# Performance work log

Measured on AMD Instinct MI355X. Metric: run time of the kernel, lower is better.

## Reference

```python
import jax, jax.numpy as jnp
import numpy as np

N = {'QENT': 20000, 'CENT': 50000, 'SPAN': 40000, 'SENT': 40000}
E = 250000
IN_DIM, HID = 256, 128
NEG_SLOPE = 0.2  # GATConv default negative_slope
RELS = [('QENT', 'SPAN'), ('QENT', 'SENT'), ('CENT', 'SENT'), ('SPAN', 'CENT'), ('CENT', 'CENT')]
ENAMES = ['e_qent_span', 'e_qent_sent', 'e_cent_sent', 'e_span_cent', 'e_cent_cooccur']


def setup_inputs() -> dict:
    key = jax.random.key(0)
    ks = jax.random.split(key, 20)
    inp = {}
    for i, t in enumerate(['QENT', 'CENT', 'SPAN', 'SENT']):
        inp['x_' + t] = jax.random.normal(ks[i], (N[t], IN_DIM), jnp.float32)
    for i, (nm, (s, d)) in enumerate(zip(ENAMES, RELS)):
        k1, k2 = jax.random.split(ks[4 + i])
        src = jax.random.randint(k1, (E,), 0, N[s])
        dst = jax.random.randint(k2, (E,), 0, N[d])
        inp[nm] = jnp.stack([src, dst]).astype(jnp.int32)
    inp['lin_W'] = jax.random.normal(ks[10], (4, IN_DIM, HID), jnp.float32) / np.sqrt(IN_DIM).astype(np.float32)
    inp['lin_b'] = jnp.zeros((4, HID), jnp.float32)
    inp['conv_Ws'] = jax.random.normal(ks[11], (2, 5, HID, HID), jnp.float32) / np.sqrt(HID).astype(np.float32)
    inp['conv_Wd'] = jax.random.normal(ks[12], (2, 5, HID, HID), jnp.float32) / np.sqrt(HID).astype(np.float32)
    inp['conv_as'] = jax.random.normal(ks[13], (2, 5, HID), jnp.float32) / np.sqrt(HID).astype(np.float32)
    inp['conv_ad'] = jax.random.normal(ks[14], (2, 5, HID), jnp.float32) / np.sqrt(HID).astype(np.float32)
    inp['conv_b'] = jnp.zeros((2, 5, HID), jnp.float32)
    inp['out_W'] = jax.random.normal(ks[15], (HID, 1), jnp.float32) / np.sqrt(HID).astype(np.float32)
    inp['out_b'] = jnp.zeros((1,), jnp.float32)
    return inp


def _gat(x_src, x_dst, edge, Ws, Wd, a_s, a_d, b, n_dst):
    """PyG GATConv, heads=1, concat=True, add_self_loops=False, bipartite lin_src/lin_dst."""
    hs = x_src @ Ws                       # [Ns, H]
    hd = x_dst @ Wd                       # [Nd, H]
    src, dst = edge[0], edge[1]
    e = jax.nn.leaky_relu((hs @ a_s)[src] + (hd @ a_d)[dst], NEG_SLOPE)  # [E]
    m = jax.ops.segment_max(e, dst, num_segments=n_dst)
    m = jnp.where(jnp.isfinite(m), m, 0.0)
    ex = jnp.exp(e - m[dst])
    denom = jax.ops.segment_sum(ex, dst, num_segments=n_dst)
    alpha = ex / (denom[dst] + 1e-16)     # segment softmax (PyG adds 1e-16)
    out = jax.ops.segment_sum(alpha[:, None] * hs[src], dst, num_segments=n_dst)
    return out + b


def _forward(x_QENT, x_CENT, x_SPAN, x_SENT,
             e_qent_span, e_qent_sent, e_cent_sent, e_span_cent, e_cent_cooccur,
             lin_W, lin_b, conv_Ws, conv_Wd, conv_as, conv_ad, conv_b, out_W, out_b):
    # per-type input projection (pyg Linear has bias)
    x = {'QENT': x_QENT @ lin_W[0] + lin_b[0],
         'CENT': x_CENT @ lin_W[1] + lin_b[1],
         'SPAN': x_SPAN @ lin_W[2] + lin_b[2],
         'SENT': x_SENT @ lin_W[3] + lin_b[3]}
    for l in range(2):
        p = lambda r: (conv_Ws[l, r], conv_Wd[l, r], conv_as[l, r], conv_ad[l, r], conv_b[l, r])
        span = _gat(x['QENT'], x['SPAN'], e_qent_span, *p(0), N['SPAN'])
        sent = (_gat(x['QENT'], x['SENT'], e_qent_sent, *p(1), N['SENT'])
                + _gat(x['CENT'], x['SENT'], e_cent_sent, *p(2), N['SENT']))  # HeteroConv aggr='sum'
        cent = (_gat(x['SPAN'], x['CENT'], e_span_cent, *p(3), N['CENT'])
                + _gat(x['CENT'], x['CENT'], e_cent_cooccur, *p(4), N['CENT']))
        x = {'QENT': x['QENT'],  # QENT has no incoming edges; carried through so layer 2 can use it as source
             'SPAN': jax.nn.relu(span),
             'SENT': jax.nn.relu(sent),
             'CENT': jax.nn.relu(cent)}
    return (x['SPAN'] @ out_W + out_b)[:, 0]  # squeeze(-1) -> [N_SPAN]


def reference(x_QENT, x_CENT, x_SPAN, x_SENT,
              e_qent_span, e_qent_sent, e_cent_sent, e_span_cent, e_cent_cooccur,
              lin_W, lin_b, conv_Ws, conv_Wd, conv_as, conv_ad, conv_b, out_W, out_b):
    return _forward(x_QENT, x_CENT, x_SPAN, x_SENT,
                    e_qent_span, e_qent_sent, e_cent_sent, e_span_cent, e_cent_cooccur,
                    lin_W, lin_b, conv_Ws, conv_Wd, conv_as, conv_ad, conv_b, out_W, out_b)
```

## Files before the change

### kernel.cpp

```cpp
#include <hip/hip_runtime.h>
#include <hip/hip_fp16.h>

#define IN_DIM 256
#define HID 128
#define ELLW 16
#define OVF_CAP 32768

using bf16x8 = __attribute__((ext_vector_type(8))) short;
using f32x4 = __attribute__((ext_vector_type(4))) float;

struct h8 { __half2 a, b, c, d; };

__device__ __forceinline__ unsigned short f2bf(float f) {
    unsigned u = __float_as_uint(f);
    u += 0x7fffu + ((u >> 16) & 1u);
    return (unsigned short)(u >> 16);
}

template <int CTRL>
__device__ __forceinline__ float dpp_rot(float x) {
    return __int_as_float(
        __builtin_amdgcn_update_dpp(0, __float_as_int(x), CTRL, 0xf, 0xf, false));
}
__device__ __forceinline__ float rsum16(float x) {
    x += dpp_rot<0x121>(x);
    x += dpp_rot<0x122>(x);
    x += dpp_rot<0x124>(x);
    x += dpp_rot<0x128>(x);
    return x;
}
__device__ __forceinline__ float rmax16(float x) {
    x = fmaxf(x, dpp_rot<0x121>(x));
    x = fmaxf(x, dpp_rot<0x122>(x));
    x = fmaxf(x, dpp_rot<0x124>(x));
    x = fmaxf(x, dpp_rot<0x128>(x));
    return x;
}

__device__ __forceinline__ float lrelu(float t) { return t > 0.f ? t : 0.2f * t; }

__device__ __forceinline__ void accum8(f32x4& a0, f32x4& a1, float a, const h8& hv) {
    const float2 f0 = __half22float2(hv.a);
    const float2 f1 = __half22float2(hv.b);
    const float2 f2 = __half22float2(hv.c);
    const float2 f3 = __half22float2(hv.d);
    a0[0] += a * f0.x; a0[1] += a * f0.y;
    a0[2] += a * f1.x; a0[3] += a * f1.y;
    a1[0] += a * f2.x; a1[1] += a * f2.y;
    a1[2] += a * f3.x; a1[3] += a * f3.y;
}

__device__ __forceinline__ float epilogue16(const f32x4& a0, const f32x4& a1,
                                            const float* __restrict__ bias,
                                            const float* __restrict__ dvec, int sl) {
    const f32x4 bb0 = *reinterpret_cast<const f32x4*>(bias + sl * 8);
    const f32x4 bb1 = *reinterpret_cast<const f32x4*>(bias + sl * 8 + 4);
    const f32x4 d0 = *reinterpret_cast<const f32x4*>(dvec + sl * 8);
    const f32x4 d1 = *reinterpret_cast<const f32x4*>(dvec + sl * 8 + 4);
    float q = 0.f;
#pragma unroll
    for (int i = 0; i < 4; ++i) {
        q += fmaxf(a0[i] + bb0[i], 0.f) * d0[i];
        q += fmaxf(a1[i] + bb1[i], 0.f) * d1[i];
    }
    return rsum16(q);
}

__global__ __launch_bounds__(256) void setup_k(const float* __restrict__ lin_W,
                                               const float* __restrict__ lin_b,
                                               const float* __restrict__ conv_Ws,
                                               const float* __restrict__ Wd,
                                               const float* __restrict__ adv,
                                               short* __restrict__ wt0,
                                               short* __restrict__ wt1,
                                               float* __restrict__ bc,
                                               float* __restrict__ wd_out,
                                               float* __restrict__ v2,
                                               float* __restrict__ c2,
                                               int* __restrict__ deg,
                                               int* __restrict__ ell,
                                               int* __restrict__ ovf_cnt, int NS, int zd) {
    const int b = blockIdx.x;
    if (b < 256) {
        const int idx = b * 256 + threadIdx.x;
        const int l = idx >> 15;
        const int rem = idx & 32767;
        const int k = rem >> 7;
        const int n = rem & 127;
        const float* lw = lin_W + (size_t)k * HID;
        const float* cw = conv_Ws + (size_t)(l * 5) * HID * HID + n;
        float s = 0.f;
#pragma unroll 4
        for (int m = 0; m < HID; ++m) s += lw[m] * cw[(size_t)m * HID];
        short* wt = l ? wt1 : wt0;
        wt[((k >> 3) << 10) + (n << 3) + (k & 7)] = (short)f2bf(s);
    } else if (b == 256) {
        const int t = threadIdx.x;
        const int l = t >> 7;
        const int n = t & 127;
        const float* cw = conv_Ws + (size_t)(l * 5) * HID * HID + n;
        float s = 0.f;
#pragma unroll 4
        for (int m = 0; m < HID; ++m) s += lin_b[m] * cw[(size_t)m * HID];
        bc[t] = s;
        if (t == 0) ovf_cnt[0] = 0;
    } else if (b == 257) {
        __shared__ float wd1s[HID];
        const int t = threadIdx.x;
        const int l = t >> 7, j = t & 127;
        const float* w = Wd + ((size_t)(l * 5) * HID + j) * HID;
        const float* a = adv + (size_t)(l * 5) * HID;
        float s = 0.f;
        for (int k = 0; k < HID; k += 4) {
            const float4 wv = *reinterpret_cast<const float4*>(w + k);
            const float4 av = *reinterpret_cast<const float4*>(a + k);
            s += wv.x * av.x + wv.y * av.y + wv.z * av.z + wv.w * av.w;
        }
        wd_out[t] = s;
        if (l == 0) wd1s[j] = s;
        __syncthreads();
        const float* wr = lin_W + 2 * (size_t)IN_DIM * HID + (size_t)t * HID;
        float p = 0.f;
        for (int k = 0; k < HID; k += 4) {
            const float4 wv = *reinterpret_cast<const float4*>(wr + k);
            p += wv.x * wd1s[k] + wv.y * wd1s[k + 1] + wv.z * wd1s[k + 2] +
                 wv.w * wd1s[k + 3];
        }
        v2[t] = p;
        if (t == 0) {
            const float* br = lin_b + 2 * HID;
            float q = 0.f;
            for (int k = 0; k < HID; ++k) q += br[k] * wd1s[k];
            c2[0] = q;
        }
    } else if (b < 258 + zd) {
        const int i4 = ((b - 258) * 256 + threadIdx.x) * 4;
        if (i4 + 4 <= NS) {
            *reinterpret_cast<int4*>(deg + i4) = make_int4(0, 0, 0, 0);
        } else {
            for (int i = i4; i < NS; ++i) deg[i] = 0;
        }
    } else {
        const int total = NS * ELLW;
        const int i4 = ((b - 258 - zd) * 256 + threadIdx.x) * 4;
        if (i4 + 4 <= total) *reinterpret_cast<int4*>(ell + i4) = make_int4(0, 0, 0, 0);
    }
}

__global__ __launch_bounds__(256) void build_gemm_k(
    const int* __restrict__ src, const int* __restrict__ dst, int E,
    int* __restrict__ deg, int* __restrict__ ell, int2* __restrict__ ovf,
    int* __restrict__ ovf_cnt, const float* __restrict__ A,
    const short* __restrict__ Wt0, const short* __restrict__ Wt1,
    const float* __restrict__ bc, __half* __restrict__ hs,
    float2* __restrict__ as12, const float* __restrict__ a1v,
    const float* __restrict__ a2v, int N, int eb) {
    if ((int)blockIdx.x < eb) {
        const int e = blockIdx.x * 256 + threadIdx.x;
        if (e < E) {
            const int d = dst[e], s = src[e];
            const int pos = atomicAdd(deg + d, 1);
            if (pos < ELLW) {
                ell[(size_t)d * ELLW + pos] = s;
            } else {
                const int oi = atomicAdd(ovf_cnt, 1);
                if (oi < OVF_CAP) ovf[oi] = make_int2(d, s);
            }
        }
        return;
    }
    const int bid = (int)blockIdx.x - eb;
    const int tid = threadIdx.x;
    const int w = tid >> 6;
    const int lane = tid & 63;
    const int m16 = lane & 15;
    const int kg = lane >> 4;

    const int arow = bid * 64 + w * 16 + m16;
    const bool ok = arow < N;

    f32x4 acc[16];
#pragma unroll
    for (int j = 0; j < 16; ++j) acc[j] = (f32x4){0.f, 0.f, 0.f, 0.f};

    for (int k0 = 0; k0 < IN_DIM; k0 += 32) {
        bf16x8 af = {0, 0, 0, 0, 0, 0, 0, 0};
        if (ok) {
            const float* ap = A + (size_t)arow * IN_DIM + k0 + kg * 8;
            const float4 f0 = *reinterpret_cast<const float4*>(ap);
            const float4 f1 = *reinterpret_cast<const float4*>(ap + 4);
            af[0] = (short)f2bf(f0.x); af[1] = (short)f2bf(f0.y);
            af[2] = (short)f2bf(f0.z); af[3] = (short)f2bf(f0.w);
            af[4] = (short)f2bf(f1.x); af[5] = (short)f2bf(f1.y);
            af[6] = (short)f2bf(f1.z); af[7] = (short)f2bf(f1.w);
        }
        const int boff = ((k0 >> 3) + kg) << 10;
        const short* b0 = Wt0 + boff;
        const short* b1 = Wt1 + boff;
#pragma unroll
        for (int j = 0; j < 8; ++j) {
            const bf16x8 bf0 = *reinterpret_cast<const bf16x8*>(b0 + ((j * 16 + m16) << 3));
            acc[j] = __builtin_amdgcn_mfma_f32_16x16x32_bf16(af, bf0, acc[j], 0, 0, 0);
            const bf16x8 bf1 = *reinterpret_cast<const bf16x8*>(b1 + ((j * 16 + m16) << 3));
            acc[j + 8] = __builtin_amdgcn_mfma_f32_16x16x32_bf16(af, bf1, acc[j + 8], 0, 0, 0);
        }
    }

    const int rbase = bid * 64 + w * 16 + kg * 4;
    float p1[4] = {0.f, 0.f, 0.f, 0.f};
    float p2[4] = {0.f, 0.f, 0.f, 0.f};
#pragma unroll
    for (int j = 0; j < 8; ++j) {
        const int col = j * 16 + m16;
        const float b0v = bc[col];
        const float b1v = bc[128 + col];
        const float a1 = a1v[col];
        const float a2 = a2v[col];
        const int so = j * 32 + ((m16 >> 3) << 4) + (m16 & 7);
#pragma unroll
        for (int r = 0; r < 4; ++r) {
            const int row = rbase + r;
            const float v1 = acc[j][r] + b0v;
            const float v2v = acc[j + 8][r] + b1v;
            if (row < N) {
                hs[(size_t)row * 256 + so] = __float2half(v1);
                hs[(size_t)row * 256 + so + 8] = __float2half(v2v);
            }
            p1[r] += v1 * a1;
            p2[r] += v2v * a2;
        }
    }
#pragma unroll
    for (int r = 0; r < 4; ++r) {
        p1[r] = rsum16(p1[r]);
        p2[r] = rsum16(p2[r]);
    }
    if (m16 == 0)
#pragma unroll
        for (int r = 0; r < 4; ++r) {
            const int row = rbase + r;
            if (row < N) as12[row] = make_float2(p1[r], p2[r]);
        }
}

__global__ __launch_bounds__(256, 4) void gat_fused_k(
    const int* __restrict__ deg_arr, const int* __restrict__ ell,
    const int2* __restrict__ ovf, const int* __restrict__ ovf_cnt_p,
    const float* __restrict__ x_span, const float* __restrict__ v2,
    const float* __restrict__ c2, const float2* __restrict__ as12,
    const __half* __restrict__ hs, const float* __restrict__ b1,
    const float* __restrict__ wd2v, const float* __restrict__ b2,
    const float* __restrict__ outW, const float* __restrict__ outb,
    float* __restrict__ out, int Ndst) {
    const int row = (blockIdx.x * blockDim.x + threadIdx.x) >> 6;
    const int lane = threadIdx.x & 63;
    const int sl = lane & 15;
    const int eg = lane >> 4;
    if (row >= Ndst) return;

    const int deg = deg_arr[row];
    const int ce = ell[(size_t)row * ELLW + sl];
    const float2 asv = as12[ce];

    const float4 xv = *reinterpret_cast<const float4*>(x_span + (size_t)row * IN_DIM +
                                                       lane * 4);
    const float4 vv = *reinterpret_cast<const float4*>(v2 + lane * 4);
    float p = xv.x * vv.x + xv.y * vv.y + xv.z * vv.z + xv.w * vv.w;
    p = rsum16(p);
    p += __shfl_xor(p, 16, 64);
    p += __shfl_xor(p, 32, 64);
    const float ad1 = p + c2[0];

    if (deg <= ELLW) {
        const float ex1 = (sl < deg) ? __expf(lrelu(asv.x + ad1)) : 0.f;
        const float al1 = ex1 / (rsum16(ex1) + 1e-16f);

        f32x4 a0 = {0.f, 0.f, 0.f, 0.f}, a1 = {0.f, 0.f, 0.f, 0.f};
        h8 h2s[4];
#pragma unroll
        for (int r = 0; r < 4; ++r) {
            if (r * 4 < deg) {
                const int e = r * 4 + eg;
                const int s = __shfl(ce, e, 64);
                const float a = __shfl(al1, e, 64);
                const __half* hb = hs + (size_t)s * 256 + sl * 16;
                const h8 hv1 = *reinterpret_cast<const h8*>(hb);
                h2s[r] = *reinterpret_cast<const h8*>(hb + 8);
                accum8(a0, a1, a, hv1);
            }
        }
#pragma unroll
        for (int i = 0; i < 4; ++i) {
            a0[i] += __shfl_xor(a0[i], 16, 64);
            a0[i] += __shfl_xor(a0[i], 32, 64);
            a1[i] += __shfl_xor(a1[i], 16, 64);
            a1[i] += __shfl_xor(a1[i], 32, 64);
        }
        const float ad2 = epilogue16(a0, a1, b1, wd2v, sl);

        const float ex2 = (sl < deg) ? __expf(lrelu(asv.y + ad2)) : 0.f;
        const float al2 = ex2 / (rsum16(ex2) + 1e-16f);

        f32x4 b0 = {0.f, 0.f, 0.f, 0.f}, b1v = {0.f, 0.f, 0.f, 0.f};
#pragma unroll
        for (int r = 0; r < 4; ++r) {
            if (r * 4 < deg) {
                const float a = __shfl(al2, r * 4 + eg, 64);
                accum8(b0, b1v, a, h2s[r]);
            }
        }
#pragma unroll
        for (int i = 0; i < 4; ++i) {
            b0[i] += __shfl_xor(b0[i], 16, 64);
            b0[i] += __shfl_xor(b0[i], 32, 64);
            b1v[i] += __shfl_xor(b1v[i], 16, 64);
            b1v[i] += __shfl_xor(b1v[i], 32, 64);
        }
        const float q = epilogue16(b0, b1v, b2, outW, sl);
        if (lane == 0) out[row] = q + outb[0];
    } else {
        int oc = *ovf_cnt_p;
        if (oc > OVF_CAP) oc = OVF_CAP;
        float ad = ad1;
#pragma unroll
        for (int layer = 0; layer < 2; ++layer) {
            const float ac = layer ? asv.y : asv.x;
            const int ho = layer ? 8 : 0;
            const float* bias = layer ? b2 : b1;
            const float* dvec = layer ? outW : wd2v;

            float te = lrelu(ac + ad);
            float m = rmax16(te);
            for (int i = 0; i < oc; ++i) {
                const int2 o = ovf[i];
                if (o.x == row) {
                    const float2 oas = as12[o.y];
                    m = fmaxf(m, lrelu((layer ? oas.y : oas.x) + ad));
                }
            }
            const float ex = __expf(te - m);
            float dsum = rsum16(ex);
            for (int i = 0; i < oc; ++i) {
                const int2 o = ovf[i];
                if (o.x == row) {
                    const float2 oas = as12[o.y];
                    dsum += __expf(lrelu((layer ? oas.y : oas.x) + ad) - m);
                }
            }
            const float inv = 1.f / (dsum + 1e-16f);
            const float al = ex * inv;

            f32x4 acc0 = {0.f, 0.f, 0.f, 0.f}, acc1 = {0.f, 0.f, 0.f, 0.f};
            for (int i = 0; i < 16; ++i) {
                const int s = __shfl(ce, i, 64);
                float a = __shfl(al, i, 64);
                if (eg != 0) a = 0.f;
                const h8 hv =
                    *reinterpret_cast<const h8*>(hs + (size_t)s * 256 + sl * 16 + ho);
                accum8(acc0, acc1, a, hv);
            }
            for (int i = 0; i < oc; ++i) {
                const int2 o = ovf[i];
                if (o.x == row && eg == 0) {
                    const float2 oas = as12[o.y];
                    const float a = __expf(lrelu((layer ? oas.y : oas.x) + ad) - m) * inv;
                    const h8 hv =
                        *reinterpret_cast<const h8*>(hs + (size_t)o.y * 256 + sl * 16 + ho);
                    accum8(acc0, acc1, a, hv);
                }
            }
#pragma unroll
            for (int i = 0; i < 4; ++i) {
                acc0[i] += __shfl_xor(acc0[i], 16, 64);
                acc0[i] += __shfl_xor(acc0[i], 32, 64);
                acc1[i] += __shfl_xor(acc1[i], 16, 64);
                acc1[i] += __shfl_xor(acc1[i], 32, 64);
            }
            const float q = epilogue16(acc0, acc1, bias, dvec, sl);
            if (layer == 0) {
                ad = q;
            } else if (lane == 0) {
                out[row] = q + outb[0];
            }
        }
    }
}

extern "C" void kernel_launch(void* const* d_in, const int* in_sizes, int n_in,
                              void* d_out, int out_size, void* d_ws, size_t ws_size,
                              hipStream_t stream) {
    const float* x_qent = (const float*)d_in[0];
    const float* x_span = (const float*)d_in[2];
    const int* e_qs = (const int*)d_in[4];
    const float* lin_W = (const float*)d_in[9];
    const float* lin_b = (const float*)d_in[10];
    const float* conv_Ws = (const float*)d_in[11];
    const float* conv_Wd = (const float*)d_in[12];
    const float* conv_as = (const float*)d_in[13];
    const float* conv_ad = (const float*)d_in[14];
    const float* conv_b = (const float*)d_in[15];
    const float* out_W = (const float*)d_in[16];
    const float* out_b = (const float*)d_in[17];

    const int NQ = in_sizes[0] / IN_DIM;
    const int NS = in_sizes[2] / IN_DIM;
    const int E = in_sizes[4] / 2;
    const int* srcp = e_qs;
    const int* dstp = e_qs + E;
    (void)n_in; (void)out_size;

    float* ws = (float*)d_ws;
    size_t off = 0;
    auto alloc = [&](size_t n) {
        n = (n + 3) & ~(size_t)3;
        float* p = ws + off;
        off += n;
        return p;
    };
    __half* hs = (__half*)alloc((size_t)NQ * 128);
    float2* as12 = (float2*)alloc(2 * (size_t)NQ);
    float* wd2 = alloc(2 * HID);
    float* v2 = alloc(IN_DIM);
    float* c2 = alloc(1);
    float* bc = alloc(2 * HID);
    int* deg = (int*)alloc(NS);
    int* ell = (int*)alloc((size_t)NS * ELLW);
    int2* ovf = (int2*)alloc(2 * OVF_CAP);
    int* ovf_cnt = (int*)alloc(1);
    short* wt0 = (short*)alloc(IN_DIM * HID / 2);
    short* wt1 = (short*)alloc(IN_DIM * HID / 2);
    (void)ws_size;

    const int zd = (NS + 1023) / 1024;
    const int ze = (NS * ELLW + 1023) / 1024;
    setup_k<<<dim3(258 + zd + ze), dim3(256), 0, stream>>>(
        lin_W, lin_b, conv_Ws, conv_Wd, conv_ad, wt0, wt1, bc, wd2, v2, c2, deg, ell,
        ovf_cnt, NS, zd);

    const int eb = (E + 255) / 256;
    const int gb = (NQ + 63) / 64;
    build_gemm_k<<<dim3(eb + gb), dim3(256), 0, stream>>>(
        srcp, dstp, E, deg, ell, ovf, ovf_cnt, x_qent, wt0, wt1, bc, hs, as12, conv_as,
        conv_as + 5 * (size_t)HID, NQ, eb);

    gat_fused_k<<<dim3(((size_t)NS * 64 + 255) / 256), dim3(256), 0, stream>>>(
        deg, ell, ovf, ovf_cnt, x_span, v2, c2, as12, hs, conv_b, wd2 + HID,
        conv_b + 5 * (size_t)HID, out_W, out_b, (float*)d_out, NS);
}
```

Measured before the change: 88.10 us.

## Move dst attention dot product into build kernel and drop ELL zeroing

The per-destination attention term (x_span·v2 + c2) is now computed by extra blocks in the build/GEMM kernel and stored to a small array, so the gather kernel no longer streams x_span rows. This lets that work overlap with edge bucketing and the GEMM. The ELL table is no longer zero-filled in setup. Instead, unused slots are masked by degree in the gather kernel, which removes a write pass of NS*16 ints. The cost is an extra global array round-trip and reliance on correct masking wherever stale ELL entries might be read.

After: 85.60 us. 2.8% less time.

```diff
diff --git a/kernel.cpp b/kernel.cpp
--- a/kernel.cpp
+++ b/kernel.cpp
@@ -78,8 +78,7 @@
                                                float* __restrict__ v2,
                                                float* __restrict__ c2,
                                                int* __restrict__ deg,
-                                               int* __restrict__ ell,
-                                               int* __restrict__ ovf_cnt, int NS, int zd) {
+                                               int* __restrict__ ovf_cnt, int NS) {
     const int b = blockIdx.x;
     if (b < 256) {
         const int idx = b * 256 + threadIdx.x;
@@ -133,17 +132,13 @@
             for (int k = 0; k < HID; ++k) q += br[k] * wd1s[k];
             c2[0] = q;
         }
-    } else if (b < 258 + zd) {
+    } else {
         const int i4 = ((b - 258) * 256 + threadIdx.x) * 4;
         if (i4 + 4 <= NS) {
             *reinterpret_cast<int4*>(deg + i4) = make_int4(0, 0, 0, 0);
         } else {
             for (int i = i4; i < NS; ++i) deg[i] = 0;
         }
-    } else {
-        const int total = NS * ELLW;
-        const int i4 = ((b - 258 - zd) * 256 + threadIdx.x) * 4;
-        if (i4 + 4 <= total) *reinterpret_cast<int4*>(ell + i4) = make_int4(0, 0, 0, 0);
     }
 }
 
@@ -154,7 +149,9 @@
     const short* __restrict__ Wt0, const short* __restrict__ Wt1,
     const float* __restrict__ bc, __half* __restrict__ hs,
     float2* __restrict__ as12, const float* __restrict__ a1v,
-    const float* __restrict__ a2v, int N, int eb) {
+    const float* __restrict__ a2v, int N, int eb,
+    const float* __restrict__ x_span, const float* __restrict__ v2,
+    const float* __restrict__ c2, float* __restrict__ ad1_out, int NS, int gb) {
     if ((int)blockIdx.x < eb) {
         const int e = blockIdx.x * 256 + threadIdx.x;
         if (e < E) {
@@ -169,6 +166,24 @@
         }
         return;
     }
+    if ((int)blockIdx.x >= eb + gb) {
+        const int idx = ((int)blockIdx.x - eb - gb) * 256 + threadIdx.x;
+        const int row = idx >> 4;
+        const int sl = threadIdx.x & 15;
+        if (row >= NS) return;
+        const float* xr = x_span + (size_t)row * IN_DIM + sl * 16;
+        const float* vr = v2 + sl * 16;
+        float p = 0.f;
+#pragma unroll
+        for (int i = 0; i < 4; ++i) {
+            const float4 xv = *reinterpret_cast<const float4*>(xr + i * 4);
+            const float4 vv = *reinterpret_cast<const float4*>(vr + i * 4);
+            p += xv.x * vv.x + xv.y * vv.y + xv.z * vv.z + xv.w * vv.w;
+        }
+        p = rsum16(p);
+        if (sl == 0) ad1_out[row] = p + c2[0];
+        return;
+    }
     const int bid = (int)blockIdx.x - eb;
     const int tid = threadIdx.x;
     const int w = tid >> 6;
@@ -246,8 +261,7 @@
 __global__ __launch_bounds__(256, 4) void gat_fused_k(
     const int* __restrict__ deg_arr, const int* __restrict__ ell,
     const int2* __restrict__ ovf, const int* __restrict__ ovf_cnt_p,
-    const float* __restrict__ x_span, const float* __restrict__ v2,
-    const float* __restrict__ c2, const float2* __restrict__ as12,
+    const float* __restrict__ ad1_arr, const float2* __restrict__ as12,
     const __half* __restrict__ hs, const float* __restrict__ b1,
     const float* __restrict__ wd2v, const float* __restrict__ b2,
     const float* __restrict__ outW, const float* __restrict__ outb,
@@ -259,17 +273,10 @@
     if (row >= Ndst) return;
 
     const int deg = deg_arr[row];
-    const int ce = ell[(size_t)row * ELLW + sl];
+    int ce = ell[(size_t)row * ELLW + sl];
+    if (sl >= deg) ce = 0;
     const float2 asv = as12[ce];
-
-    const float4 xv = *reinterpret_cast<const float4*>(x_span + (size_t)row * IN_DIM +
-                                                       lane * 4);
-    const float4 vv = *reinterpret_cast<const float4*>(v2 + lane * 4);
-    float p = xv.x * vv.x + xv.y * vv.y + xv.z * vv.z + xv.w * vv.w;
-    p = rsum16(p);
-    p += __shfl_xor(p, 16, 64);
-    p += __shfl_xor(p, 32, 64);
-    const float ad1 = p + c2[0];
+    const float ad1 = ad1_arr[row];
 
     if (deg <= ELLW) {
         const float ex1 = (sl < deg) ? __expf(lrelu(asv.x + ad1)) : 0.f;
@@ -419,6 +426,7 @@
     };
     __half* hs = (__half*)alloc((size_t)NQ * 128);
     float2* as12 = (float2*)alloc(2 * (size_t)NQ);
+    float* ad1 = alloc(NS);
     float* wd2 = alloc(2 * HID);
     float* v2 = alloc(IN_DIM);
     float* c2 = alloc(1);
@@ -432,18 +440,18 @@
     (void)ws_size;
 
     const int zd = (NS + 1023) / 1024;
-    const int ze = (NS * ELLW + 1023) / 1024;
-    setup_k<<<dim3(258 + zd + ze), dim3(256), 0, stream>>>(
-        lin_W, lin_b, conv_Ws, conv_Wd, conv_ad, wt0, wt1, bc, wd2, v2, c2, deg, ell,
-        ovf_cnt, NS, zd);
+    setup_k<<<dim3(258 + zd), dim3(256), 0, stream>>>(
+        lin_W, lin_b, conv_Ws, conv_Wd, conv_ad, wt0, wt1, bc, wd2, v2, c2, deg, ovf_cnt,
+        NS);
 
     const int eb = (E + 255) / 256;
     const int gb = (NQ + 63) / 64;
-    build_gemm_k<<<dim3(eb + gb), dim3(256), 0, stream>>>(
+    const int ab = ((size_t)NS * 16 + 255) / 256;
+    build_gemm_k<<<dim3(eb + gb + ab), dim3(256), 0, stream>>>(
         srcp, dstp, E, deg, ell, ovf, ovf_cnt, x_qent, wt0, wt1, bc, hs, as12, conv_as,
-        conv_as + 5 * (size_t)HID, NQ, eb);
+        conv_as + 5 * (size_t)HID, NQ, eb, x_span, v2, c2, ad1, NS, gb);
 
     gat_fused_k<<<dim3(((size_t)NS * 64 + 255) / 256), dim3(256), 0, stream>>>(
-        deg, ell, ovf, ovf_cnt, x_span, v2, c2, as12, hs, conv_b, wd2 + HID,
+        deg, ell, ovf, ovf_cnt, ad1, as12, hs, conv_b, wd2 + HID,
         conv_b + 5 * (size_t)HID, out_W, out_b, (float*)d_out, NS);
 }
```
